# Kernel optimization log

Hardware: AMD Instinct MI355X
Metric: run time of the kernel (lower is better)

The kernel has to match this reference:

```python
import jax, jax.numpy as jnp
import numpy as np

# ---- static circuit configuration (matches module init) ----
C = 6        # Fock cutoff (strawberryfields.tf cutoff_dim)
N = 5        # modes / wires
OUTPUT = 2   # output_size
LAYERS = 4   # layers
M = N * (N - 1) + max(1, N - 1)  # 24: params per interferometer

# ladder operators in truncated Fock basis
_a = np.diag(np.sqrt(np.arange(1, C)), 1)
A = jnp.asarray(_a, dtype=jnp.complex64)          # annihilation
AD = A.conj().T                                    # creation
NUM = jnp.arange(C, dtype=jnp.float32)             # number operator diag
I1 = jnp.eye(C, dtype=jnp.complex64)
A1 = jnp.kron(A, I1)   # a on mode 1 of a 2-mode block
A2 = jnp.kron(I1, A)   # a on mode 2 of a 2-mode block


def _expm(H, order=16, s=6):
    # scaling-and-squaring + Horner Taylor; fully differentiable, small matrices only
    Hs = H * jnp.asarray(1.0 / (2 ** s), H.dtype)
    I = jnp.eye(H.shape[-1], dtype=H.dtype)
    R = I
    for k in range(order, 0, -1):
        R = I + (Hs @ R) * jnp.asarray(1.0 / k, H.dtype)
    for _ in range(s):
        R = R @ R
    return R


def disp_gate(r, phi):
    al = jax.lax.complex(r * jnp.cos(phi), r * jnp.sin(phi))
    return _expm(al * AD - jnp.conj(al) * A)


def squeeze_gate(r):
    # S(r, 0) = exp(r/2 (a^2 - adag^2))
    return _expm(jax.lax.complex(r, jnp.zeros_like(r)) * 0.5 * (A @ A - AD @ AD))


def rot_gate(phi):
    return jnp.diag(jnp.exp(1j * phi * NUM))


def kerr_gate(kap):
    return jnp.diag(jnp.exp(1j * kap * NUM * NUM))


def bs_gate(theta, phi):
    ep = jnp.exp(1j * phi)
    H = ep * (A1 @ A2.conj().T) - jnp.conj(ep) * (A1.conj().T @ A2)
    th = jax.lax.complex(theta, jnp.zeros_like(theta))
    return _expm(th * H).reshape(C, C, C, C)


def apply1(U, psi, m):
    psi = jnp.tensordot(U, psi, axes=([1], [m]))
    return jnp.moveaxis(psi, 0, m)


def apply2(U4, psi, m):
    # U4[o1,o2,i1,i2] acting on adjacent modes (m, m+1)
    psi = jnp.tensordot(U4, psi, axes=([2, 3], [m, m + 1]))
    return jnp.moveaxis(psi, [0, 1], [m, m + 1])


def interferometer(p, psi):
    T = N * (N - 1) // 2
    theta, phi, rphi = p[:T], p[T:2 * T], p[-(N - 1):]
    n = 0
    for l in range(N):
        for k in range(N - 1):
            if (l + k) % 2 == 0:  # same condition as (l+k)%2 != 1 being False
                psi = apply2(bs_gate(theta[n], phi[n]), psi, k)
                n += 1
    for i in range(max(1, N - 1)):
        psi = apply1(rot_gate(rphi[i]), psi, i)
    return psi


def linear_layer(p, psi):
    psi = interferometer(p[:M], psi)
    for i in range(N):
        psi = apply1(squeeze_gate(p[M + i]), psi, i)
    psi = interferometer(p[M + N:2 * M + N], psi)
    dr = p[2 * M + N:2 * M + 2 * N]
    dp = p[2 * M + 2 * N:2 * M + 3 * N]
    for i in range(N):
        psi = apply1(disp_gate(dr[i], dp[i]), psi, i)
    return psi


def circuit(xi, lin, act, last_act):
    psi = jnp.zeros((C,) * N, jnp.complex64).at[(0,) * N].set(1.0)
    zero = jnp.float32(0.0)
    for i in range(N):  # Displacement encoding of input
        psi = apply1(disp_gate(xi[i], zero), psi, i)
    for l in range(LAYERS - 1):
        psi = linear_layer(lin[l], psi)
        for i in range(N):  # Kerr activation
            psi = apply1(kerr_gate(act[l, i]), psi, i)
    psi = linear_layer(lin[LAYERS - 1], psi)
    for i in range(OUTPUT):  # last activation on first OUTPUT modes
        psi = apply1(kerr_gate(last_act[i]), psi, i)
    X = A + AD  # x quadrature, hbar=2 (StrawberryFields convention)
    return jnp.stack([jnp.real(jnp.vdot(psi, apply1(X, psi, i))) for i in range(OUTPUT)])


def setup_inputs() -> dict:
    key = jax.random.key(0)
    k1, k2, k3, k4 = jax.random.split(key, 4)
    B = 2048
    x = jax.random.uniform(k1, (B, N), dtype=jnp.float32)
    linear_params = 0.001 * jax.random.normal(k2, (LAYERS, 2 * M + 3 * N), dtype=jnp.float32)
    activation_params = 0.001 * jax.random.normal(k3, (LAYERS - 1, N), dtype=jnp.float32)
    last_activation_params = 0.001 * jax.random.normal(k4, (N,), dtype=jnp.float32)
    return {
        "x": x,
        "linear_params": linear_params,
        "activation_params": activation_params,
        "last_activation_params": last_activation_params,
    }


def reference(x, linear_params, activation_params, last_activation_params):
    f = lambda xi: circuit(xi, linear_params, activation_params, last_activation_params)
    return jax.vmap(f)(x)  # [B, OUTPUT]
```

## Files before the change

### kernel.cpp

```cpp
#include <hip/hip_runtime.h>


typedef float    vf2 __attribute__((ext_vector_type(2)));
typedef _Float16 h2  __attribute__((ext_vector_type(2)));
typedef _Float16 h4  __attribute__((ext_vector_type(4)));

__device__ __forceinline__ h2 pkfma(const h2 a, const h2 b, const h2 c) {
    return __builtin_elementwise_fma(a, b, c);
}

__device__ __forceinline__ void cmadd(float &ax, float &ay, const float2 u, const float2 v) {
    ax = fmaf(u.x, v.x, ax);
    ax = fmaf(-u.y, v.y, ax);
    ay = fmaf(u.x, v.y, ay);
    ay = fmaf(u.y, v.x, ay);
}

constexpr int BS_SN[11]  = {1,2,3,4,5,6,5,4,3,2,1};
constexpr int BS_OFF[11] = {0,1,5,14,30,55,91,116,132,141,145};

__device__ const int d_BS_OFF[12] = {0,1,5,14,30,55,91,116,132,141,145,146};
__device__ const int d_BS_SN[11]  = {1,2,3,4,5,6,5,4,3,2,1};

__global__ void gates_kernel(const float* __restrict__ lin,
                             const float* __restrict__ act,
                             const float* __restrict__ lact,
                             h2* __restrict__ bsh,
                             h2* __restrict__ sgh)
{
    __shared__ float2 B0[1296];
    __shared__ float2 B1[1296];
    const int tid = threadIdx.x;

    if (blockIdx.x < 80) {
        const int g = blockIdx.x;
        const int l = g / 20;
        const int w = g % 20;
        const int q = w / 10;
        const int n = w % 10;
        const float theta = lin[l*63 + (q ? 29 : 0) + n];
        const float phi   = lin[l*63 + (q ? 39 : 10) + n];
        const float ts = theta * 0.015625f;
        const float cp = cosf(phi), sp = sinf(phi);
        const float2 u  = make_float2( ts*cp, ts*sp);
        const float2 w2 = make_float2(-ts*cp, ts*sp);

        float2 *R = B0, *T = B1;
        for (int e = tid; e < 1296; e += 256)
            R[e] = make_float2((e % 37 == 0) ? 1.f : 0.f, 0.f);
        __syncthreads();

        for (int k = 16; k >= 1; --k) {
            const float invk = 1.f / (float)k;
            for (int e = tid; e < 1296; e += 256) {
                const int row = e / 36, c = e - row*36;
                const int i = row / 6, j = row - (row/6)*6;
                float ax = 0.f, ay = 0.f;
                if (i < 5 && j > 0) {
                    const float coef = sqrtf((float)((i+1)*j));
                    const float2 x = R[(row+5)*36 + c];
                    const float px = u.x*x.x - u.y*x.y;
                    const float py = u.x*x.y + u.y*x.x;
                    ax = fmaf(coef, px, ax); ay = fmaf(coef, py, ay);
                }
                if (i > 0 && j < 5) {
                    const float coef = sqrtf((float)(i*(j+1)));
                    const float2 x = R[(row-5)*36 + c];
                    const float px = w2.x*x.x - w2.y*x.y;
                    const float py = w2.x*x.y + w2.y*x.x;
                    ax = fmaf(coef, px, ax); ay = fmaf(coef, py, ay);
                }
                T[e] = make_float2(((row == c) ? 1.f : 0.f) + ax*invk, ay*invk);
            }
            __syncthreads();
            float2* tmp = R; R = T; T = tmp;
        }
        for (int s2 = 0; s2 < 6; ++s2) {
            for (int e = tid; e < 1296; e += 256) {
                const int row = e / 36, c = e - row*36;
                float ax = 0.f, ay = 0.f;
                #pragma unroll 6
                for (int k = 0; k < 36; ++k)
                    cmadd(ax, ay, R[row*36 + k], R[k*36 + c]);
                T[e] = make_float2(ax, ay);
            }
            __syncthreads();
            float2* tmp = R; R = T; T = tmp;
        }
        for (int idx = tid; idx < 146; idx += 256) {
            int nn = 0;
            while (idx >= d_BS_OFF[nn+1]) ++nn;
            const int sn  = d_BS_SN[nn];
            const int rel = idx - d_BS_OFF[nn];
            const int p = rel / sn, qq = rel % sn;
            const int imin = (nn > 5) ? (nn - 5) : 0;
            const int row = 5*(imin + p)  + nn;
            const int col = 5*(imin + qq) + nn;
            const float2 z = R[row*36 + col];
            bsh[g*292 + 2*idx    ] = (h2){(_Float16)z.x, (_Float16)z.x};
            bsh[g*292 + 2*idx + 1] = (h2){(_Float16)z.y, (_Float16)z.y};
        }
    } else {
        const int t = tid;
        if (t >= 40) return;
        const int l  = t / 10;
        const int gi = t % 10;
        float2 G[36];
        if (gi < 5) {
            const int m = gi;
            const float r    = lin[l*63 + 24 + m];
            const float rphi = (m < 4) ? lin[l*63 + 20 + m] : 0.f;
            float R[36], T[36];
            #pragma unroll
            for (int e = 0; e < 36; ++e) R[e] = (e % 7 == 0) ? 1.f : 0.f;
            float hp[4];
            #pragma unroll
            for (int i = 0; i < 4; ++i)
                hp[i] = 0.5f * r * sqrtf((float)((i+1)*(i+2))) * 0.015625f;
            for (int k = 16; k >= 1; --k) {
                const float invk = 1.f / (float)k;
                #pragma unroll
                for (int i = 0; i < 6; ++i) {
                    #pragma unroll
                    for (int c = 0; c < 6; ++c) {
                        float a = 0.f;
                        if (i < 4)  a = fmaf( hp[i],   R[(i+2)*6 + c], a);
                        if (i >= 2) a = fmaf(-hp[i-2], R[(i-2)*6 + c], a);
                        T[i*6+c] = ((i == c) ? 1.f : 0.f) + a*invk;
                    }
                }
                #pragma unroll
                for (int e = 0; e < 36; ++e) R[e] = T[e];
            }
            for (int s2 = 0; s2 < 6; ++s2) {
                #pragma unroll
                for (int i = 0; i < 6; ++i) {
                    #pragma unroll
                    for (int c = 0; c < 6; ++c) {
                        float a = 0.f;
                        #pragma unroll
                        for (int k = 0; k < 6; ++k) a = fmaf(R[i*6+k], R[k*6+c], a);
                        T[i*6+c] = a;
                    }
                }
                #pragma unroll
                for (int e = 0; e < 36; ++e) R[e] = T[e];
            }
            #pragma unroll
            for (int c = 0; c < 6; ++c) {
                const float cc = cosf(rphi * (float)c), ss = sinf(rphi * (float)c);
                #pragma unroll
                for (int o = 0; o < 6; ++o)
                    G[o*6 + c] = make_float2(R[o*6+c]*cc, R[o*6+c]*ss);
            }
        } else {
            const int m = gi - 5;
            const float dr   = lin[l*63 + 53 + m];
            const float dp   = lin[l*63 + 58 + m];
            const float rphi = (m < 4) ? lin[l*63 + 49 + m] : 0.f;
            const float kap  = (l < 3) ? act[l*5 + m] : ((m < 2) ? lact[m] : 0.f);
            const float2 al = make_float2(dr * cosf(dp), dr * sinf(dp));
            float2 R[36], T[36];
            #pragma unroll
            for (int e = 0; e < 36; ++e)
                R[e] = make_float2((e % 7 == 0) ? 1.f : 0.f, 0.f);
            float2 cm[6], cpb[6];
            #pragma unroll
            for (int i = 0; i < 6; ++i) {
                const float sm  = sqrtf((float)i)     * 0.015625f;
                const float sp2 = sqrtf((float)(i+1)) * 0.015625f;
                cm[i]  = make_float2( al.x*sm,  al.y*sm);
                cpb[i] = make_float2(-al.x*sp2, al.y*sp2);
            }
            for (int k = 16; k >= 1; --k) {
                const float invk = 1.f / (float)k;
                #pragma unroll
                for (int i = 0; i < 6; ++i) {
                    #pragma unroll
                    for (int c = 0; c < 6; ++c) {
                        float ax = 0.f, ay = 0.f;
                        if (i >= 1) cmadd(ax, ay, cm[i],  R[(i-1)*6 + c]);
                        if (i < 5)  cmadd(ax, ay, cpb[i], R[(i+1)*6 + c]);
                        T[i*6+c] = make_float2(((i == c) ? 1.f : 0.f) + ax*invk, ay*invk);
                    }
                }
                #pragma unroll
                for (int e = 0; e < 36; ++e) R[e] = T[e];
            }
            for (int s2 = 0; s2 < 6; ++s2) {
                #pragma unroll
                for (int i = 0; i < 6; ++i) {
                    #pragma unroll
                    for (int c = 0; c < 6; ++c) {
                        float ax = 0.f, ay = 0.f;
                        #pragma unroll
                        for (int k = 0; k < 6; ++k) cmadd(ax, ay, R[i*6+k], R[k*6+c]);
                        T[i*6+c] = make_float2(ax, ay);
                    }
                }
                #pragma unroll
                for (int e = 0; e < 36; ++e) R[e] = T[e];
            }
            #pragma unroll
            for (int o = 0; o < 6; ++o) {
                const float ko = kap * (float)(o*o);
                const float2 kp = make_float2(cosf(ko), sinf(ko));
                #pragma unroll
                for (int c = 0; c < 6; ++c) {
                    const float rc = rphi * (float)c;
                    const float2 rp = make_float2(cosf(rc), sinf(rc));
                    const float2 z = R[o*6 + c];
                    const float2 t1 = make_float2(kp.x*z.x - kp.y*z.y, kp.x*z.y + kp.y*z.x);
                    G[o*6 + c] = make_float2(t1.x*rp.x - t1.y*rp.y, t1.x*rp.y + t1.y*rp.x);
                }
            }
        }
        h2* outp = sgh + (l*10 + gi)*72;
        #pragma unroll
        for (int e = 0; e < 36; ++e) {
            outp[2*e    ] = (h2){(_Float16)G[e].x, (_Float16)G[e].x};
            outp[2*e + 1] = (h2){(_Float16)G[e].y, (_Float16)G[e].y};
        }
    }
}

__global__ void dcol_kernel(const float* __restrict__ x,
                            float* __restrict__ dcol, const int total)
{
    const int i = blockIdx.x * 256 + threadIdx.x;
    if (i >= total) return;
    const float xv = x[i];
    float a[5];
    #pragma unroll
    for (int j = 0; j < 5; ++j) a[j] = xv * sqrtf((float)(j+1)) * 0.015625f;
    float R[36], T[36];
    #pragma unroll
    for (int e = 0; e < 36; ++e) R[e] = (e % 7 == 0) ? 1.f : 0.f;
    for (int k = 16; k >= 1; --k) {
        const float invk = 1.f / (float)k;
        #pragma unroll
        for (int r = 0; r < 6; ++r) {
            #pragma unroll
            for (int c = 0; c < 6; ++c) {
                float acc = 0.f;
                if (r >= 1) acc = fmaf( a[r-1], R[(r-1)*6 + c], acc);
                if (r < 5)  acc = fmaf(-a[r],   R[(r+1)*6 + c], acc);
                T[r*6+c] = ((r == c) ? 1.f : 0.f) + acc*invk;
            }
        }
        #pragma unroll
        for (int e = 0; e < 36; ++e) R[e] = T[e];
    }
    for (int s2 = 0; s2 < 6; ++s2) {
        #pragma unroll
        for (int r = 0; r < 6; ++r) {
            #pragma unroll
            for (int c = 0; c < 6; ++c) {
                float acc = 0.f;
                #pragma unroll
                for (int k = 0; k < 6; ++k) acc = fmaf(R[r*6+k], R[k*6+c], acc);
                T[r*6+c] = acc;
            }
        }
        #pragma unroll
        for (int e = 0; e < 36; ++e) R[e] = T[e];
    }
    #pragma unroll
    for (int j = 0; j < 6; ++j) dcol[i*6 + j] = R[j*6 + 0];
}


template<int SA, int SB, int n, int R0, int R1>
__device__ __forceinline__ void bs_rows(const h2* __restrict__ U,
                                        h4* __restrict__ psi,
                                        const int base, const bool act)
{
    constexpr int sn = BS_SN[n], uoff = BS_OFF[n];
    constexpr int imin = (n > 5) ? (n - 5) : 0;
    if (!act) return;
    h2 vR[sn], vI[sn];
    #pragma unroll
    for (int q = 0; q < sn; ++q) {
        const int c = 5*(imin + q) + n;
        const h4 v = psi[base + (c/6)*SA + (c%6)*SB];
        vR[q] = (h2){v.x, v.y};
        vI[q] = (h2){v.z, v.w};
    }
    h2 oR[R1-R0], oI[R1-R0];
    #pragma unroll
    for (int p = R0; p < R1; ++p) {
        const h2* Up = U + 2*(uoff + p*sn);
        h2 ur = Up[0], ui = Up[1];
        h2 aR = ur * vR[0];
        aR = pkfma(-ui, vI[0], aR);
        h2 aI = ur * vI[0];
        aI = pkfma(ui, vR[0], aI);
        #pragma unroll
        for (int q = 1; q < sn; ++q) {
            ur = Up[2*q]; ui = Up[2*q + 1];
            aR = pkfma(ur, vR[q], aR);
            aR = pkfma(-ui, vI[q], aR);
            aI = pkfma(ur, vI[q], aI);
            aI = pkfma(ui, vR[q], aI);
        }
        oR[p-R0] = aR; oI[p-R0] = aI;
    }
    #pragma unroll
    for (int p = R0; p < R1; ++p) {
        const int c = 5*(imin + p) + n;
        const h2 r = oR[p-R0], m = oI[p-R0];
        psi[base + (c/6)*SA + (c%6)*SB] = (h4){r.x, r.y, m.x, m.y};
    }
}

template<int SA, int SB>
__device__ __forceinline__ void pass_bs(const h2* __restrict__ U,
                                        h4* __restrict__ psi,
                                        const int base, const bool act, const int qid)
{
    if (qid == 0) {
        bs_rows<SA,SB,5,0,6>(U, psi, base, act);
    } else if (qid == 1) {
        bs_rows<SA,SB,4,0,5>(U, psi, base, act);
        bs_rows<SA,SB,2,0,3>(U, psi, base, act);
        bs_rows<SA,SB,1,0,2>(U, psi, base, act);
    } else if (qid == 2) {
        bs_rows<SA,SB,6,0,5>(U, psi, base, act);
        bs_rows<SA,SB,8,0,3>(U, psi, base, act);
        bs_rows<SA,SB,9,0,2>(U, psi, base, act);
    } else {
        bs_rows<SA,SB,3,0,4>(U, psi, base, act);
        bs_rows<SA,SB,7,0,4>(U, psi, base, act);
        bs_rows<SA,SB,0,0,1>(U, psi, base, act);
        bs_rows<SA,SB,10,0,1>(U, psi, base, act);
    }
    __syncthreads();
}

template<int SM, bool SP>
__device__ __forceinline__ void sg_fiber(const h2* __restrict__ G,
                                         h4* __restrict__ psi,
                                         const int base)
{
    h2 vR[6], vI[6];
    #pragma unroll
    for (int k = 0; k < 6; ++k) {
        const h4 v = psi[base + k*SM];
        vR[k] = (h2){v.x, v.y};
        vI[k] = (h2){v.z, v.w};
    }
    h2 oR[6], oI[6];
    #pragma unroll
    for (int o = 0; o < 6; ++o) {
        const int k0 = SP ? (o & 1) : 0;
        const int st = SP ? 2 : 1;
        h2 ur = G[2*(o*6 + k0)], ui = G[2*(o*6 + k0) + 1];
        h2 aR = ur * vR[k0];
        aR = pkfma(-ui, vI[k0], aR);
        h2 aI = ur * vI[k0];
        aI = pkfma(ui, vR[k0], aI);
        #pragma unroll
        for (int k = k0 + st; k < 6; k += st) {
            ur = G[2*(o*6 + k)]; ui = G[2*(o*6 + k) + 1];
            aR = pkfma(ur, vR[k], aR);
            aR = pkfma(-ui, vI[k], aR);
            aI = pkfma(ur, vI[k], aI);
            aI = pkfma(ui, vR[k], aI);
        }
        oR[o] = aR; oI[o] = aI;
    }
    #pragma unroll
    for (int o = 0; o < 6; ++o)
        psi[base + o*SM] = (h4){oR[o].x, oR[o].y, oI[o].x, oI[o].y};
}

template<int SM, int S0, int S1, int S2, int S3, bool SP>
__device__ __forceinline__ void pass_sg(const h2* __restrict__ G,
                                        h4* __restrict__ psi,
                                        const int4 dg0, const int4 dg1, const bool act1)
{
    {
        const int base = dg0.x*S0 + dg0.y*S1 + dg0.z*S2 + dg0.w*S3;
        sg_fiber<SM,SP>(G, psi, base);
    }
    if (act1) {
        const int base = dg1.x*S0 + dg1.y*S1 + dg1.z*S2 + dg1.w*S3;
        sg_fiber<SM,SP>(G, psi, base);
    }
    __syncthreads();
}

__global__ __launch_bounds__(1024, 8)
void qnet_kernel(const h2* __restrict__ bs,
                 const h2* __restrict__ sg,
                 const float* __restrict__ dcol,
                 float* __restrict__ out,
                 const int B)
{
    __shared__ __align__(16) h4 psi[7992];
    __shared__ float stf[60];
    __shared__ float red[64];

    const int tid = threadIdx.x;
    const int b   = blockIdx.x;

    const int lim = B * 30;
    if (tid < 60) stf[tid] = (b*60 + tid < lim) ? dcol[b*60 + tid] : 0.f;
    __syncthreads();
    for (int e = tid; e < 7776; e += 1024) {
        int t = e;
        const int i4 = t % 6; t /= 6;
        const int i3 = t % 6; t /= 6;
        const int i2 = t % 6; t /= 6;
        const int i1 = t % 6; t /= 6;
        const int i0 = t;
        const int addr = 6*i0 + i1 + 36*i2 + 221*i3 + 1334*i4;
        const float v0 = stf[i0]*stf[6+i1]*stf[12+i2]*stf[18+i3]*stf[24+i4];
        const float v1 = stf[30+i0]*stf[36+i1]*stf[42+i2]*stf[48+i3]*stf[54+i4];
        psi[addr] = (h4){(_Float16)v0, (_Float16)v1, (_Float16)0.f, (_Float16)0.f};
    }
    __syncthreads();

    const int sub = tid & 255;
    const int qid = __builtin_amdgcn_readfirstlane(tid >> 8);
    const bool act = sub < 216;
    const int f = act ? sub : 215;
    const int fa = f / 36, rem = f - fa*36;
    const int fb = rem / 6, fc = rem - fb*6;
    const int baseK0 = fa*36 + fb*221 + fc*1334;
    const int baseK1 = fa*6  + fb*221 + fc*1334;
    const int baseK2 = rem   + fa*1334;
    const int baseK3 = f;

    int4 dg0, dg1;
    { int t = tid;        dg0.x = t % 6; t /= 6; dg0.y = t % 6; t /= 6; dg0.z = t % 6; dg0.w = t / 6; }
    { int t = tid + 1024; dg1.x = t % 6; t /= 6; dg1.y = t % 6; t /= 6; dg1.z = t % 6; dg1.w = t / 6; }
    const bool act1 = tid < 272;

    for (int l = 0; l < 4; ++l) {
        const h2* bsl = bs + l * 20 * 292;
        const h2* sgl = sg + l * 10 * 72;
        for (int hf = 0; hf < 2; ++hf) {
            const h2* bh = bsl + hf * 10 * 292;
            const h2* sh = sgl + hf * 5 * 72;
            const bool last = (l == 3) && (hf == 1);
            pass_bs<6,1>     (bh + 0*292, psi, baseK0, act, qid);
            pass_bs<36,221>  (bh + 1*292, psi, baseK2, act, qid);
            pass_bs<1,36>    (bh + 2*292, psi, baseK1, act, qid);
            pass_bs<221,1334>(bh + 3*292, psi, baseK3, act, qid);
            pass_bs<6,1>     (bh + 4*292, psi, baseK0, act, qid);
            pass_bs<36,221>  (bh + 5*292, psi, baseK2, act, qid);
            pass_bs<1,36>    (bh + 6*292, psi, baseK1, act, qid);
            if (!last)
                pass_bs<221,1334>(bh + 7*292, psi, baseK3, act, qid);
            pass_bs<6,1>     (bh + 8*292, psi, baseK0, act, qid);
            if (!last)
                pass_bs<36,221>  (bh + 9*292, psi, baseK2, act, qid);
            if (hf == 0) {
                pass_sg<6,    1,36,221,1334, true>(sh + 0*72, psi, dg0, dg1, act1);
                pass_sg<1,    6,36,221,1334, true>(sh + 1*72, psi, dg0, dg1, act1);
                pass_sg<36,   1,6,221,1334,  true>(sh + 2*72, psi, dg0, dg1, act1);
                pass_sg<221,  1,6,36,1334,   true>(sh + 3*72, psi, dg0, dg1, act1);
                pass_sg<1334, 1,6,36,221,    true>(sh + 4*72, psi, dg0, dg1, act1);
            } else {
                pass_sg<6,    1,36,221,1334, false>(sh + 0*72, psi, dg0, dg1, act1);
                pass_sg<1,    6,36,221,1334, false>(sh + 1*72, psi, dg0, dg1, act1);
                if (!last) {
                    pass_sg<36,   1,6,221,1334,  false>(sh + 2*72, psi, dg0, dg1, act1);
                    pass_sg<221,  1,6,36,1334,   false>(sh + 3*72, psi, dg0, dg1, act1);
                    pass_sg<1334, 1,6,36,221,    false>(sh + 4*72, psi, dg0, dg1, act1);
                }
            }
        }
    }

    float s0a = 0.f, s0b = 0.f, s1a = 0.f, s1b = 0.f;
    for (int fr = tid; fr < 1296; fr += 1024) {
        const int q0 = fr % 6;
        const int q1 = (fr / 6) % 6;
        const int q2 = (fr / 36) % 6;
        const int q3 = fr / 216;
        const int base0 = q0*1 + q1*36 + q2*221 + q3*1334;
        #pragma unroll
        for (int j = 0; j < 5; ++j) {
            const h4 a = psi[base0 + 6*j];
            const h4 c = psi[base0 + 6*(j+1)];
            const float w = sqrtf((float)(j+1));
            s0a = fmaf(w, fmaf((float)a.z, (float)c.z, (float)a.x*(float)c.x), s0a);
            s0b = fmaf(w, fmaf((float)a.w, (float)c.w, (float)a.y*(float)c.y), s0b);
        }
        const int base1 = q0*6 + q1*36 + q2*221 + q3*1334;
        #pragma unroll
        for (int j = 0; j < 5; ++j) {
            const h4 a = psi[base1 + j];
            const h4 c = psi[base1 + j + 1];
            const float w = sqrtf((float)(j+1));
            s1a = fmaf(w, fmaf((float)a.z, (float)c.z, (float)a.x*(float)c.x), s1a);
            s1b = fmaf(w, fmaf((float)a.w, (float)c.w, (float)a.y*(float)c.y), s1b);
        }
    }
    #pragma unroll
    for (int off = 32; off > 0; off >>= 1) {
        s0a += __shfl_down(s0a, off, 64);
        s0b += __shfl_down(s0b, off, 64);
        s1a += __shfl_down(s1a, off, 64);
        s1b += __shfl_down(s1b, off, 64);
    }
    if ((tid & 63) == 0) {
        const int w = tid >> 6;
        red[w*4 + 0] = s0a; red[w*4 + 1] = s1a;
        red[w*4 + 2] = s0b; red[w*4 + 3] = s1b;
    }
    __syncthreads();
    if (tid == 0) {
        float r0 = 0.f, r1 = 0.f, r2 = 0.f, r3 = 0.f;
        #pragma unroll
        for (int w = 0; w < 16; ++w) {
            r0 += red[w*4 + 0]; r1 += red[w*4 + 1];
            r2 += red[w*4 + 2]; r3 += red[w*4 + 3];
        }
        const int b0 = 2*b, b1 = 2*b + 1;
        out[b0*2 + 0] = 2.f * r0;
        out[b0*2 + 1] = 2.f * r1;
        if (b1 < B) {
            out[b1*2 + 0] = 2.f * r2;
            out[b1*2 + 1] = 2.f * r3;
        }
    }
}

extern "C" void kernel_launch(void* const* d_in, const int* in_sizes, int n_in,
                              void* d_out, int out_size, void* d_ws, size_t ws_size,
                              hipStream_t stream)
{
    const float* x    = (const float*)d_in[0];
    const float* lin  = (const float*)d_in[1];
    const float* act  = (const float*)d_in[2];
    const float* lact = (const float*)d_in[3];
    float* out = (float*)d_out;

    const int B = in_sizes[0] / 5;

    h2*    bsh = (h2*)d_ws;
    h2*    sgh = bsh + 80*292;
    float* dc  = (float*)(sgh + 40*72);

    gates_kernel<<<dim3(81), dim3(256), 0, stream>>>(lin, act, lact, bsh, sgh);
    const int total = B * 5;
    dcol_kernel<<<dim3((total + 255)/256), dim3(256), 0, stream>>>(x, dc, total);
    qnet_kernel<<<dim3((B + 1) / 2), dim3(1024), 0, stream>>>(bsh, sgh, dc, out, B);
}
```

Measured before the change: 782.1 us.

## Fold first three beamsplitter passes into product-state initialization

The initial state is a product state, so the first beamsplitters on modes (0,1), (2,3) and then (3,4) are applied analytically to small per-mode factors in fp32 before the full 6^5 state is built. The state is then formed as an outer product of a 36-entry and a 216-entry complex factor, and three full-state beamsplitter passes in the first half-layer are skipped. This removes three shared-memory sweeps with their barriers, at the cost of a few small prologue steps and extra shared arrays. Correctness relies on the beamsplitter ordering allowing the (3,4) gate to act before the (1,2) gate.

```diff
diff --git a/kernel.cpp b/kernel.cpp
--- a/kernel.cpp
+++ b/kernel.cpp
@@ -400,6 +400,9 @@
     __shared__ __align__(16) h4 psi[7992];
     __shared__ float stf[60];
     __shared__ float red[64];
+    __shared__ float2 ps01[2][36];
+    __shared__ float2 ps23[2][36];
+    __shared__ float2 f234[2][216];
 
     const int tid = threadIdx.x;
     const int b   = blockIdx.x;
@@ -407,6 +410,54 @@
     const int lim = B * 30;
     if (tid < 60) stf[tid] = (b*60 + tid < lim) ? dcol[b*60 + tid] : 0.f;
     __syncthreads();
+
+    if (tid < 144) {
+        const int part = tid / 36;
+        const int idx  = tid - part*36;
+        const int p    = part & 1;
+        const bool m01 = part < 2;
+        const int i = idx / 6, j = idx - (idx/6)*6;
+        const int n = i + j;
+        const int imin = (n > 5) ? (n - 5) : 0;
+        const int sn   = d_BS_SN[n];
+        const int prow = i - imin;
+        const h2* U = bs + (m01 ? 0 : 1)*292 + 2*(d_BS_OFF[n] + prow*sn);
+        const float* dA = stf + p*30 + (m01 ? 0 : 12);
+        const float* dB = dA + 6;
+        float ar = 0.f, ai = 0.f;
+        for (int q = 0; q < sn; ++q) {
+            const float ur = (float)U[2*q].x, ui = (float)U[2*q+1].x;
+            const float dd = dA[imin+q] * dB[n-imin-q];
+            ar = fmaf(ur, dd, ar); ai = fmaf(ui, dd, ai);
+        }
+        if (m01) ps01[p][idx] = make_float2(ar, ai);
+        else     ps23[p][idx] = make_float2(ar, ai);
+    }
+    __syncthreads();
+
+    if (tid < 432) {
+        const int p  = tid / 216;
+        const int r  = tid - p*216;
+        const int i2 = r / 36, i34 = r - i2*36;
+        const int i3 = i34 / 6, i4 = i34 - i3*6;
+        const int n  = i3 + i4;
+        const int imin = (n > 5) ? (n - 5) : 0;
+        const int sn   = d_BS_SN[n];
+        const int prow = i3 - imin;
+        const h2* U = bs + 3*292 + 2*(d_BS_OFF[n] + prow*sn);
+        const float* d4 = stf + p*30 + 24;
+        float ar = 0.f, ai = 0.f;
+        for (int q = 0; q < sn; ++q) {
+            const float ur = (float)U[2*q].x, ui = (float)U[2*q+1].x;
+            const float2 w23 = ps23[p][i2*6 + (imin+q)];
+            const float dd = d4[n-imin-q];
+            ar = fmaf(dd, ur*w23.x - ui*w23.y, ar);
+            ai = fmaf(dd, ur*w23.y + ui*w23.x, ai);
+        }
+        f234[p][r] = make_float2(ar, ai);
+    }
+    __syncthreads();
+
     for (int e = tid; e < 7776; e += 1024) {
         int t = e;
         const int i4 = t % 6; t /= 6;
@@ -415,9 +466,13 @@
         const int i1 = t % 6; t /= 6;
         const int i0 = t;
         const int addr = 6*i0 + i1 + 36*i2 + 221*i3 + 1334*i4;
-        const float v0 = stf[i0]*stf[6+i1]*stf[12+i2]*stf[18+i3]*stf[24+i4];
-        const float v1 = stf[30+i0]*stf[36+i1]*stf[42+i2]*stf[48+i3]*stf[54+i4];
-        psi[addr] = (h4){(_Float16)v0, (_Float16)v1, (_Float16)0.f, (_Float16)0.f};
+        const int i01 = i0*6 + i1;
+        const int r   = i2*36 + i3*6 + i4;
+        const float2 a0 = ps01[0][i01], b0 = f234[0][r];
+        const float2 a1 = ps01[1][i01], b1 = f234[1][r];
+        const float v0r = a0.x*b0.x - a0.y*b0.y, v0i = a0.x*b0.y + a0.y*b0.x;
+        const float v1r = a1.x*b1.x - a1.y*b1.y, v1i = a1.x*b1.y + a1.y*b1.x;
+        psi[addr] = (h4){(_Float16)v0r, (_Float16)v1r, (_Float16)v0i, (_Float16)v1i};
     }
     __syncthreads();
 
@@ -443,11 +498,15 @@
         for (int hf = 0; hf < 2; ++hf) {
             const h2* bh = bsl + hf * 10 * 292;
             const h2* sh = sgl + hf * 5 * 72;
+            const bool first = (l == 0) && (hf == 0);
             const bool last = (l == 3) && (hf == 1);
-            pass_bs<6,1>     (bh + 0*292, psi, baseK0, act, qid);
-            pass_bs<36,221>  (bh + 1*292, psi, baseK2, act, qid);
+            if (!first) {
+                pass_bs<6,1>     (bh + 0*292, psi, baseK0, act, qid);
+                pass_bs<36,221>  (bh + 1*292, psi, baseK2, act, qid);
+            }
             pass_bs<1,36>    (bh + 2*292, psi, baseK1, act, qid);
-            pass_bs<221,1334>(bh + 3*292, psi, baseK3, act, qid);
+            if (!first)
+                pass_bs<221,1334>(bh + 3*292, psi, baseK3, act, qid);
             pass_bs<6,1>     (bh + 4*292, psi, baseK0, act, qid);
             pass_bs<36,221>  (bh + 5*292, psi, baseK2, act, qid);
             pass_bs<1,36>    (bh + 6*292, psi, baseK1, act, qid);
```

Result: no change. 771.4 us (-1.4%).
